# Optimization experiments

Hardware: AMD Instinct MI355X
Metric: run time of the kernel (lower is better)

Reference implementation:

```python
import jax, jax.numpy as jnp
import numpy as np

B, S, D, H = 2, 2048, 1024, 16
HD = D // H          # head dim = 64
BASE = 10000.0
SCALE = 1.0 / np.sqrt(HD)


def setup_inputs() -> dict:
    key = jax.random.key(0)
    ks = jax.random.split(key, 7)
    mk = lambda k, shp: (jax.random.normal(k, shp, dtype=jnp.float32) * 0.02)
    return {
        "hidden_states": jax.random.normal(ks[0], (B, S, D), dtype=jnp.float32),
        "Wq": mk(ks[1], (D, D)), "bq": jnp.zeros((D,), jnp.float32),
        "Wk": mk(ks[2], (D, D)), "bk": jnp.zeros((D,), jnp.float32),
        "Wv": mk(ks[3], (D, D)), "bv": jnp.zeros((D,), jnp.float32),
    }


def _rope_tables(seq_len, head_dim, dtype):
    # Intended RoPE: inv_freq over head_dim/2 frequencies.
    # (Original torch code has an off-by-2 indexing bug that makes it un-runnable
    #  for head_dim > 2; we implement the intended standard RoPE:
    #  inv_freq = base^{-arange(0, head_dim, 2)/head_dim}, length head_dim//2.)
    dim_half = head_dim // 2
    inv_freq = 1.0 / (BASE ** (jnp.arange(dim_half, dtype=dtype) / dim_half))
    ang = jnp.arange(seq_len, dtype=dtype)[:, None] * inv_freq[None, :]  # [S, dim_half]
    return jnp.sin(ang), jnp.cos(ang)


def _apply_rope(x, sin, cos):
    # x: [B, H, S, HD]; sin/cos: [S, HD//2]
    dim_half = x.shape[-1] // 2
    x1, x2 = x[..., :dim_half], x[..., dim_half:]
    sin = sin[None, None]  # [1,1,S,dim_half]
    cos = cos[None, None]
    return jnp.concatenate([x1 * cos - x2 * sin, x1 * sin + x2 * cos], axis=-1)


def reference(hidden_states, Wq, bq, Wk, bk, Wv, bv):
    b, s, d = hidden_states.shape
    # QKV projections (nn.Linear: x @ W.T + b), then split heads -> [B,H,S,HD]
    def proj(W, bias):
        y = jnp.einsum("bsd,ed->bse", hidden_states, W) + bias
        return y.reshape(b, s, H, HD).transpose(0, 2, 1, 3)

    q, k, v = proj(Wq, bq), proj(Wk, bk), proj(Wv, bv)

    sin, cos = _rope_tables(s, HD, hidden_states.dtype)
    q = _apply_rope(q, sin, cos)
    k = _apply_rope(k, sin, cos)

    # Non-causal SDPA, scale = 1/sqrt(head_dim), no mask, eval mode (no dropout)
    scores = jnp.einsum("bhqd,bhkd->bhqk", q, k) * SCALE
    probs = jax.nn.softmax(scores, axis=-1)
    ctx = jnp.einsum("bhqk,bhkd->bhqd", probs, v)

    # [B,H,S,HD] -> [B,S,D]
    return ctx.transpose(0, 2, 1, 3).reshape(b, s, d)
```

## Files before the change

kernel.cpp:

```cpp
#include <hip/hip_runtime.h>
#include <hip/hip_bf16.h>
#include <math.h>

#define B_  2
#define S_  2048
#define D_  1024
#define H_  16
#define HD_ 64
#define M_  (B_*S_)
#define N3  (3*D_)
#define K_  D_
#define LOG2E 1.44269504088896340736f

typedef unsigned short u16;
typedef __bf16 bf16x8 __attribute__((ext_vector_type(8)));
typedef float  f32x4  __attribute__((ext_vector_type(4)));
typedef float  f32x16 __attribute__((ext_vector_type(16)));
typedef unsigned short u16x4 __attribute__((ext_vector_type(4)));
typedef unsigned short u16x8 __attribute__((ext_vector_type(8)));
typedef unsigned int   u32x4v __attribute__((ext_vector_type(4)));

typedef const __attribute__((address_space(1))) unsigned int gu32;
typedef __attribute__((address_space(3)))       unsigned int lu32;

__device__ __forceinline__ void gload_lds16(const void* g, void* l) {
  __builtin_amdgcn_global_load_lds((gu32*)g, (lu32*)l, 16, 0, 0);
}

__device__ __forceinline__ u16 f2bf(float f) {
  unsigned u = __builtin_bit_cast(unsigned, f);
  u += 0x7fffu + ((u >> 16) & 1u);
  return (u16)(u >> 16);
}

__device__ __forceinline__ unsigned pk2(float lo, float hi) {
  unsigned d;
  asm("v_cvt_pk_bf16_f32 %0, %1, %2" : "=v"(d) : "v"(lo), "v"(hi));
  return d;
}

#define NPREP ((M_*D_/4 + 3*(D_*D_/4)) / 256)
__global__ void k_prep(const float* __restrict__ hs, const float* __restrict__ Wq,
                       const float* __restrict__ Wk, const float* __restrict__ Wv,
                       u16* __restrict__ Xb, u16* __restrict__ Wb,
                       float* __restrict__ sinT, float* __restrict__ cosT) {
  const int NX = M_*D_/4, NW = D_*D_/4, NTOT = NX + 3*NW;
  int i = blockIdx.x * blockDim.x + threadIdx.x;
  if (i < NTOT) {
    const float4* src; u16* dst; int off;
    if (i < NX)            { src = (const float4*)hs; dst = Xb;           off = i; }
    else if (i < NX+NW)    { src = (const float4*)Wq; dst = Wb;           off = i-NX; }
    else if (i < NX+2*NW)  { src = (const float4*)Wk; dst = Wb + D_*D_;   off = i-NX-NW; }
    else                   { src = (const float4*)Wv; dst = Wb + 2*D_*D_; off = i-NX-2*NW; }
    float4 v = src[off];
    ushort4 o; o.x = f2bf(v.x); o.y = f2bf(v.y); o.z = f2bf(v.z); o.w = f2bf(v.w);
    reinterpret_cast<ushort4*>(dst)[off] = o;
  } else {
    int gid = i - NTOT;
    int s = gid >> 5, j = gid & 31;
    float invf = (float)exp(-(double)j * (log(10000.0) / 32.0));
    float angf = (float)s * invf;
    double ang = (double)angf;
    sinT[gid] = (float)sin(ang);
    cosT[gid] = (float)cos(ang);
  }
}

#define BM 128
#define BN 128
#define BK 64

__global__ __launch_bounds__(256) void k_gemm(const u16* __restrict__ A,
                                              const u16* __restrict__ Bm,
                                              const float* __restrict__ bq,
                                              const float* __restrict__ bk,
                                              const float* __restrict__ bv,
                                              const float* __restrict__ sinT,
                                              const float* __restrict__ cosT,
                                              u16* __restrict__ Qo,
                                              u16* __restrict__ Ko,
                                              u16* __restrict__ Vt) {
  __shared__ alignas(16) u16 As[2][BM*BK];
  __shared__ alignas(16) u16 Bs[2][BN*BK];
  const int t = threadIdx.x;
  const int l = t & 63, w = t >> 6;
  const int wr = w >> 1, wc = w & 1;
  const int lr = l & 15, lg = l >> 4;

  const int lin = blockIdx.y * (N3/BN) + blockIdx.x;
  const int wk  = (lin & 7) * 96 + (lin >> 3);
  const int m0 = (wk / (N3/BN)) * BM, n0 = (wk % (N3/BN)) * BN;

  const u16* asrc[4]; const u16* bsrc[4];
#pragma unroll
  for (int i = 0; i < 4; ++i) {
    int chunk = i*256 + t;
    int row = chunk >> 3, kc = (chunk & 7) ^ (row & 7);
    asrc[i] = A  + (size_t)(m0+row)*K_ + kc*8;
    bsrc[i] = Bm + (size_t)(n0+row)*K_ + kc*8;
  }

  f32x4 acc[4][4] = {};

#pragma unroll
  for (int i = 0; i < 4; ++i) {
    int chunk = i*256 + t;
    gload_lds16(asrc[i], &As[0][chunk*8]);
    gload_lds16(bsrc[i], &Bs[0][chunk*8]);
  }
  __syncthreads();

  int cur = 0;
  for (int k0 = 0; k0 < K_; k0 += BK) {
    if (k0 + BK < K_) {
#pragma unroll
      for (int i = 0; i < 4; ++i) {
        int chunk = i*256 + t;
        gload_lds16(asrc[i] + k0 + BK, &As[cur^1][chunk*8]);
        gload_lds16(bsrc[i] + k0 + BK, &Bs[cur^1][chunk*8]);
      }
    }
#pragma unroll
    for (int ks = 0; ks < 2; ++ks) {
      bf16x8 a[4], b[4];
#pragma unroll
      for (int m = 0; m < 4; ++m) {
        int row = wr*64 + m*16 + lr;
        int g   = (ks*4 + lg) ^ (row & 7);
        a[m] = *reinterpret_cast<const bf16x8*>(&As[cur][row*BK + g*8]);
      }
#pragma unroll
      for (int n = 0; n < 4; ++n) {
        int row = wc*64 + n*16 + lr;
        int g   = (ks*4 + lg) ^ (row & 7);
        b[n] = *reinterpret_cast<const bf16x8*>(&Bs[cur][row*BK + g*8]);
      }
#pragma unroll
      for (int m = 0; m < 4; ++m)
#pragma unroll
        for (int n = 0; n < 4; ++n)
          acc[m][n] = __builtin_amdgcn_mfma_f32_16x16x32_bf16(a[m], b[n], acc[m][n], 0, 0, 0);
    }
    __syncthreads();
    cur ^= 1;
  }

  const int cw0  = n0 + wc*64;
  const int proj = cw0 >> 10;
  const int h    = (cw0 & (D_-1)) >> 6;
  const int b    = m0 >> 11;
  const int sb_  = (m0 & (S_-1)) + wr*64;

  if (proj < 2) {
    const float* bias = proj ? bk : bq;
    u16* dst = proj ? Ko : Qo;
    const float qs = proj ? 1.0f : 0.125f * LOG2E;
    float b1[2], b2[2];
#pragma unroll
    for (int n = 0; n < 2; ++n) {
      b1[n] = bias[h*HD_ + n*16 + lr];
      b2[n] = bias[h*HD_ + n*16 + lr + 32];
    }
#pragma unroll
    for (int m = 0; m < 4; ++m)
#pragma unroll
      for (int r = 0; r < 4; ++r) {
        int s = sb_ + m*16 + lg*4 + r;
        size_t orow = ((size_t)(b*H_ + h)*S_ + s)*HD_;
#pragma unroll
        for (int n = 0; n < 2; ++n) {
          int j = n*16 + lr;
          float x1 = acc[m][n][r]   + b1[n];
          float x2 = acc[m][n+2][r] + b2[n];
          float c  = cosT[(s<<5) + j], sn = sinT[(s<<5) + j];
          dst[orow + j]      = f2bf((x1*c - x2*sn) * qs);
          dst[orow + j + 32] = f2bf((x1*sn + x2*c) * qs);
        }
      }
  } else {
    float bb[4];
#pragma unroll
    for (int n = 0; n < 4; ++n) bb[n] = bv[h*HD_ + n*16 + lr];
    const int lgp = ((lg & 1) << 1) | (lg >> 1);
    const int pos0 = sb_ + lgp*4;
#pragma unroll
    for (int m = 0; m < 4; ++m)
#pragma unroll
      for (int n = 0; n < 4; ++n) {
        int hd = n*16 + lr;
        u16x4 o;
#pragma unroll
        for (int r = 0; r < 4; ++r) o[r] = f2bf(acc[m][n][r] + bb[n]);
        *reinterpret_cast<u16x4*>(Vt + ((size_t)(b*H_ + h)*HD_ + hd)*S_ + pos0 + m*16) = o;
      }
  }
}

#define QBW 32
#define NWV 4
#define QTT (QBW*NWV)
#define KTL 128
#define NTL (S_/KTL)

__global__ __launch_bounds__(256) void k_attn(const u16* __restrict__ Q,
                                              const u16* __restrict__ K,
                                              const u16* __restrict__ Vt,
                                              float* __restrict__ out) {
  __shared__ alignas(16) u16 Ks[2][KTL*HD_];
  __shared__ alignas(16) u16 Vs[2][HD_*KTL];
  __shared__ float lsums[NWV][QBW];
  const int t = threadIdx.x, l = t & 63, w = t >> 6;
  const int q32 = l & 31, hi = l >> 5;

  const int bid = blockIdx.x;
  const int work = (bid & 7) * 64 + (bid >> 3);
  const int bh = work >> 4;
  const int q0 = (work & 15) * QTT;

  const u16* Qg = Q  + ((size_t)bh*S_ + q0 + w*QBW)*HD_;
  const u16* Kg = K  + (size_t)bh*S_*HD_;
  const u16* Vg = Vt + (size_t)bh*HD_*S_;

  bf16x8 qf[4];
#pragma unroll
  for (int kt = 0; kt < 4; ++kt)
    qf[kt] = *reinterpret_cast<const bf16x8*>(Qg + (size_t)q32*HD_ + kt*16 + hi*8);

  f32x16 O0 = {}, O1 = {};
  float lp0 = 0.f, lp1 = 0.f, lp2 = 0.f, lp3 = 0.f;

  const u16* ksrc[4]; const u16* vsrc[4];
#pragma unroll
  for (int i = 0; i < 4; ++i) {
    int g  = t + 256*i;
    int kr = g >> 3,  kc = (g & 7)  ^ (kr & 7);
    ksrc[i] = Kg + (size_t)kr*HD_ + kc*8;
    int vr = g >> 4,  vc = (g & 15) ^ (vr & 15);
    vsrc[i] = Vg + (size_t)vr*S_ + vc*8;
  }

#pragma unroll
  for (int i = 0; i < 4; ++i) {
    gload_lds16(ksrc[i], &Ks[0][(t + 256*i)*8]);
    gload_lds16(vsrc[i], &Vs[0][(t + 256*i)*8]);
  }
  __syncthreads();

  int cur = 0;
  for (int tile = 0; tile < NTL; ++tile) {
    if (tile + 1 < NTL) {
#pragma unroll
      for (int i = 0; i < 4; ++i) {
        gload_lds16(ksrc[i] + (size_t)(tile+1)*KTL*HD_, &Ks[cur^1][(t + 256*i)*8]);
        gload_lds16(vsrc[i] + (tile+1)*KTL,             &Vs[cur^1][(t + 256*i)*8]);
      }
    }

#pragma unroll
    for (int half = 0; half < 2; ++half) {
      f32x16 d0 = {}, d1 = {};
      __builtin_amdgcn_s_setprio(1);
#pragma unroll
      for (int kt = 0; kt < 4; ++kt) {
        const int gsw = ((kt*2 + hi) ^ (q32 & 7)) * 8;
        bf16x8 k0 = *reinterpret_cast<const bf16x8*>(&Ks[cur][(half*64 + q32)*HD_ + gsw]);
        d0 = __builtin_amdgcn_mfma_f32_32x32x16_bf16(k0, qf[kt], d0, 0, 0, 0);
        bf16x8 k1 = *reinterpret_cast<const bf16x8*>(&Ks[cur][(half*64 + 32 + q32)*HD_ + gsw]);
        d1 = __builtin_amdgcn_mfma_f32_32x32x16_bf16(k1, qf[kt], d1, 0, 0, 0);
      }
      __builtin_amdgcn_s_setprio(0);

      unsigned pw[4][4];
#pragma unroll
      for (int c = 0; c < 4; ++c) {
        float e[8];
#pragma unroll
        for (int i = 0; i < 8; ++i) {
          float sv = (c < 2) ? d0[(c & 1)*8 + i] : d1[(c & 1)*8 + i];
          e[i] = __builtin_amdgcn_exp2f(sv);
        }
        lp0 += e[0] + e[4];
        lp1 += e[1] + e[5];
        lp2 += e[2] + e[6];
        lp3 += e[3] + e[7];
#pragma unroll
        for (int j = 0; j < 4; ++j) pw[c][j] = pk2(e[2*j], e[2*j+1]);
      }

      __builtin_amdgcn_s_setprio(1);
#pragma unroll
      for (int c = 0; c < 4; ++c) {
        u32x4v pv_ = {pw[c][0], pw[c][1], pw[c][2], pw[c][3]};
        bf16x8 pa = __builtin_bit_cast(bf16x8, pv_);
        const int gv = ((half*8 + c*2 + hi) ^ (q32 & 15)) * 8;
        bf16x8 v0 = *reinterpret_cast<const bf16x8*>(&Vs[cur][q32*KTL + gv]);
        O0 = __builtin_amdgcn_mfma_f32_32x32x16_bf16(pa, v0, O0, 0, 0, 0);
        bf16x8 v1 = *reinterpret_cast<const bf16x8*>(&Vs[cur][(32 + q32)*KTL + gv]);
        O1 = __builtin_amdgcn_mfma_f32_32x32x16_bf16(pa, v1, O1, 0, 0, 0);
      }
      __builtin_amdgcn_s_setprio(0);
    }

    __syncthreads();
    cur ^= 1;
  }

  float lsum = (lp0 + lp1) + (lp2 + lp3);
  lsum += __shfl_xor(lsum, 32);
  if (l < 32) lsums[w][l] = lsum;

  const int b = bh >> 4, h = bh & 15;
#pragma unroll
  for (int r = 0; r < 16; ++r) {
    int qrow = (r & 3) + 8*(r >> 2) + 4*hi;
    float inv = 1.f / lsums[w][qrow];
    size_t o = (size_t)(b*S_ + q0 + w*QBW + qrow)*D_ + h*HD_;
    out[o + q32]      = O0[r] * inv;
    out[o + 32 + q32] = O1[r] * inv;
  }
}

extern "C" void kernel_launch(void* const* d_in, const int* in_sizes, int n_in,
                              void* d_out, int out_size, void* d_ws, size_t ws_size,
                              hipStream_t stream) {
  const float* hs = (const float*)d_in[0];
  const float* Wq = (const float*)d_in[1];
  const float* bq = (const float*)d_in[2];
  const float* Wk = (const float*)d_in[3];
  const float* bk = (const float*)d_in[4];
  const float* Wv = (const float*)d_in[5];
  const float* bv = (const float*)d_in[6];
  float* out = (float*)d_out;

  char* ws = (char*)d_ws;
  u16*   Xb   = (u16*)  (ws);
  u16*   Wb   = (u16*)  (ws + 8388608);
  u16*   Qb   = (u16*)  (ws + 14680064);
  u16*   Kb   = (u16*)  (ws + 23068672);
  u16*   Vtb  = (u16*)  (ws + 31457280);
  float* sinT = (float*)(ws + 39845888);
  float* cosT = (float*)(ws + 40108032);

  k_prep<<<NPREP + 256, 256, 0, stream>>>(hs, Wq, Wk, Wv, Xb, Wb, sinT, cosT);
  k_gemm<<<dim3(N3/BN, M_/BM), 256, 0, stream>>>(Xb, Wb, bq, bk, bv, sinT, cosT, Qb, Kb, Vtb);
  k_attn<<<512, 256, 0, stream>>>(Qb, Kb, Vtb, out);
}
```

Measured before the change: 172.7 us.

## Split attention over two key halves with a separate reduction kernel

Attention work is split across two key/value halves, doubling the grid to 1024 blocks. Each block handles 1024 keys in 64-wide tiles with a new LDS swizzle, and writes unnormalised partial outputs and row sums. A new reduction kernel adds the two partials and divides by the combined sum. The aim is more parallelism and occupancy (launch bounds 4, smaller LDS), at the cost of an extra full-size fp32 output round trip and one more launch. The RoPE table computation also switches from double to single-precision sin and cos.

```diff
diff --git a/kernel.cpp b/kernel.cpp
--- a/kernel.cpp
+++ b/kernel.cpp
@@ -59,10 +59,9 @@
     int gid = i - NTOT;
     int s = gid >> 5, j = gid & 31;
     float invf = (float)exp(-(double)j * (log(10000.0) / 32.0));
-    float angf = (float)s * invf;
-    double ang = (double)angf;
-    sinT[gid] = (float)sin(ang);
-    cosT[gid] = (float)cos(ang);
+    float ang  = (float)s * invf;
+    sinT[gid] = sinf(ang);
+    cosT[gid] = cosf(ang);
   }
 }
 
@@ -199,27 +198,29 @@
 #define QBW 32
 #define NWV 4
 #define QTT (QBW*NWV)
-#define KTL 128
-#define NTL (S_/KTL)
-
-__global__ __launch_bounds__(256) void k_attn(const u16* __restrict__ Q,
-                                              const u16* __restrict__ K,
-                                              const u16* __restrict__ Vt,
-                                              float* __restrict__ out) {
+#define KTL 64
+#define NTL 16
+
+__global__ __launch_bounds__(256, 4) void k_attn(const u16* __restrict__ Q,
+                                                 const u16* __restrict__ K,
+                                                 const u16* __restrict__ Vt,
+                                                 float* __restrict__ out,
+                                                 float* __restrict__ Op2,
+                                                 float* __restrict__ Lp) {
   __shared__ alignas(16) u16 Ks[2][KTL*HD_];
   __shared__ alignas(16) u16 Vs[2][HD_*KTL];
-  __shared__ float lsums[NWV][QBW];
   const int t = threadIdx.x, l = t & 63, w = t >> 6;
   const int q32 = l & 31, hi = l >> 5;
 
   const int bid = blockIdx.x;
-  const int work = (bid & 7) * 64 + (bid >> 3);
-  const int bh = work >> 4;
+  const int work = (bid & 7) * 128 + (bid >> 3);
+  const int bh = work >> 5;
+  const int ks = (work >> 4) & 1;
   const int q0 = (work & 15) * QTT;
 
   const u16* Qg = Q  + ((size_t)bh*S_ + q0 + w*QBW)*HD_;
-  const u16* Kg = K  + (size_t)bh*S_*HD_;
-  const u16* Vg = Vt + (size_t)bh*HD_*S_;
+  const u16* Kg = K  + ((size_t)bh*S_ + ks*1024)*HD_;
+  const u16* Vg = Vt + (size_t)bh*HD_*S_ + ks*1024;
 
   bf16x8 qf[4];
 #pragma unroll
@@ -229,77 +230,77 @@
   f32x16 O0 = {}, O1 = {};
   float lp0 = 0.f, lp1 = 0.f, lp2 = 0.f, lp3 = 0.f;
 
-  const u16* ksrc[4]; const u16* vsrc[4];
-#pragma unroll
-  for (int i = 0; i < 4; ++i) {
+  const u16 *ksrc[2], *vsrc[2];
+#pragma unroll
+  for (int i = 0; i < 2; ++i) {
     int g  = t + 256*i;
-    int kr = g >> 3,  kc = (g & 7)  ^ (kr & 7);
-    ksrc[i] = Kg + (size_t)kr*HD_ + kc*8;
-    int vr = g >> 4,  vc = (g & 15) ^ (vr & 15);
-    vsrc[i] = Vg + (size_t)vr*S_ + vc*8;
-  }
-
-#pragma unroll
-  for (int i = 0; i < 4; ++i) {
+    int r_ = g >> 4;
+    int kg = (g & 15) ^ (r_ & 15);
+    ksrc[i] = Kg + (size_t)(r_*2 + (kg >> 3))*HD_ + (kg & 7)*8;
+    vsrc[i] = Vg + (size_t)(r_*2 + (kg >> 3))*S_  + (kg & 7)*8;
+  }
+
+#pragma unroll
+  for (int i = 0; i < 2; ++i) {
     gload_lds16(ksrc[i], &Ks[0][(t + 256*i)*8]);
     gload_lds16(vsrc[i], &Vs[0][(t + 256*i)*8]);
   }
   __syncthreads();
+
+  const int rk = q32 >> 1;
+  const int kb = (q32 & 1) << 3;
 
   int cur = 0;
   for (int tile = 0; tile < NTL; ++tile) {
     if (tile + 1 < NTL) {
 #pragma unroll
-      for (int i = 0; i < 4; ++i) {
+      for (int i = 0; i < 2; ++i) {
         gload_lds16(ksrc[i] + (size_t)(tile+1)*KTL*HD_, &Ks[cur^1][(t + 256*i)*8]);
         gload_lds16(vsrc[i] + (tile+1)*KTL,             &Vs[cur^1][(t + 256*i)*8]);
       }
     }
 
-#pragma unroll
-    for (int half = 0; half < 2; ++half) {
-      f32x16 d0 = {}, d1 = {};
-      __builtin_amdgcn_s_setprio(1);
-#pragma unroll
-      for (int kt = 0; kt < 4; ++kt) {
-        const int gsw = ((kt*2 + hi) ^ (q32 & 7)) * 8;
-        bf16x8 k0 = *reinterpret_cast<const bf16x8*>(&Ks[cur][(half*64 + q32)*HD_ + gsw]);
-        d0 = __builtin_amdgcn_mfma_f32_32x32x16_bf16(k0, qf[kt], d0, 0, 0, 0);
-        bf16x8 k1 = *reinterpret_cast<const bf16x8*>(&Ks[cur][(half*64 + 32 + q32)*HD_ + gsw]);
-        d1 = __builtin_amdgcn_mfma_f32_32x32x16_bf16(k1, qf[kt], d1, 0, 0, 0);
-      }
-      __builtin_amdgcn_s_setprio(0);
-
-      unsigned pw[4][4];
-#pragma unroll
-      for (int c = 0; c < 4; ++c) {
-        float e[8];
-#pragma unroll
-        for (int i = 0; i < 8; ++i) {
-          float sv = (c < 2) ? d0[(c & 1)*8 + i] : d1[(c & 1)*8 + i];
-          e[i] = __builtin_amdgcn_exp2f(sv);
-        }
-        lp0 += e[0] + e[4];
-        lp1 += e[1] + e[5];
-        lp2 += e[2] + e[6];
-        lp3 += e[3] + e[7];
-#pragma unroll
-        for (int j = 0; j < 4; ++j) pw[c][j] = pk2(e[2*j], e[2*j+1]);
-      }
-
-      __builtin_amdgcn_s_setprio(1);
-#pragma unroll
-      for (int c = 0; c < 4; ++c) {
-        u32x4v pv_ = {pw[c][0], pw[c][1], pw[c][2], pw[c][3]};
-        bf16x8 pa = __builtin_bit_cast(bf16x8, pv_);
-        const int gv = ((half*8 + c*2 + hi) ^ (q32 & 15)) * 8;
-        bf16x8 v0 = *reinterpret_cast<const bf16x8*>(&Vs[cur][q32*KTL + gv]);
-        O0 = __builtin_amdgcn_mfma_f32_32x32x16_bf16(pa, v0, O0, 0, 0, 0);
-        bf16x8 v1 = *reinterpret_cast<const bf16x8*>(&Vs[cur][(32 + q32)*KTL + gv]);
-        O1 = __builtin_amdgcn_mfma_f32_32x32x16_bf16(pa, v1, O1, 0, 0, 0);
-      }
-      __builtin_amdgcn_s_setprio(0);
-    }
+    f32x16 d0 = {}, d1 = {};
+    __builtin_amdgcn_s_setprio(1);
+#pragma unroll
+    for (int kt = 0; kt < 4; ++kt) {
+      const int g0 = (kb | (kt*2 + hi)) ^ rk;
+      bf16x8 k0 = *reinterpret_cast<const bf16x8*>(&Ks[cur][(rk*16 + g0)*8]);
+      d0 = __builtin_amdgcn_mfma_f32_32x32x16_bf16(k0, qf[kt], d0, 0, 0, 0);
+      bf16x8 k1 = *reinterpret_cast<const bf16x8*>(&Ks[cur][((16 + rk)*16 + g0)*8]);
+      d1 = __builtin_amdgcn_mfma_f32_32x32x16_bf16(k1, qf[kt], d1, 0, 0, 0);
+    }
+    __builtin_amdgcn_s_setprio(0);
+
+    unsigned pw[4][4];
+#pragma unroll
+    for (int c = 0; c < 4; ++c) {
+      float e[8];
+#pragma unroll
+      for (int i = 0; i < 8; ++i) {
+        float sv = (c < 2) ? d0[(c & 1)*8 + i] : d1[(c & 1)*8 + i];
+        e[i] = __builtin_amdgcn_exp2f(sv);
+      }
+      lp0 += e[0] + e[4];
+      lp1 += e[1] + e[5];
+      lp2 += e[2] + e[6];
+      lp3 += e[3] + e[7];
+#pragma unroll
+      for (int j = 0; j < 4; ++j) pw[c][j] = pk2(e[2*j], e[2*j+1]);
+    }
+
+    __builtin_amdgcn_s_setprio(1);
+#pragma unroll
+    for (int c = 0; c < 4; ++c) {
+      u32x4v pv_ = {pw[c][0], pw[c][1], pw[c][2], pw[c][3]};
+      bf16x8 pa = __builtin_bit_cast(bf16x8, pv_);
+      const int gv = (kb | (c*2 + hi)) ^ rk;
+      bf16x8 v0 = *reinterpret_cast<const bf16x8*>(&Vs[cur][(rk*16 + gv)*8]);
+      O0 = __builtin_amdgcn_mfma_f32_32x32x16_bf16(pa, v0, O0, 0, 0, 0);
+      bf16x8 v1 = *reinterpret_cast<const bf16x8*>(&Vs[cur][((16 + rk)*16 + gv)*8]);
+      O1 = __builtin_amdgcn_mfma_f32_32x32x16_bf16(pa, v1, O1, 0, 0, 0);
+    }
+    __builtin_amdgcn_s_setprio(0);
 
     __syncthreads();
     cur ^= 1;
@@ -307,17 +308,33 @@
 
   float lsum = (lp0 + lp1) + (lp2 + lp3);
   lsum += __shfl_xor(lsum, 32);
-  if (l < 32) lsums[w][l] = lsum;
-
+  if (l < 32) Lp[ks*65536 + bh*2048 + q0 + w*QBW + l] = lsum;
+
+  float* Od = ks ? Op2 : out;
   const int b = bh >> 4, h = bh & 15;
 #pragma unroll
   for (int r = 0; r < 16; ++r) {
     int qrow = (r & 3) + 8*(r >> 2) + 4*hi;
-    float inv = 1.f / lsums[w][qrow];
     size_t o = (size_t)(b*S_ + q0 + w*QBW + qrow)*D_ + h*HD_;
-    out[o + q32]      = O0[r] * inv;
-    out[o + 32 + q32] = O1[r] * inv;
-  }
+    Od[o + q32]      = O0[r];
+    Od[o + 32 + q32] = O1[r];
+  }
+}
+
+__global__ __launch_bounds__(256) void k_red(float* __restrict__ out,
+                                             const float* __restrict__ Op2,
+                                             const float* __restrict__ Lp) {
+  int i4 = blockIdx.x * 256 + threadIdx.x;
+  float4 a = reinterpret_cast<const float4*>(out)[i4];
+  float4 b = reinterpret_cast<const float4*>(Op2)[i4];
+  int bs = i4 >> 8;
+  int h  = (i4 & 255) >> 4;
+  int li = ((bs >> 11)*16 + h)*2048 + (bs & 2047);
+  float inv = 1.f / (Lp[li] + Lp[65536 + li]);
+  float4 r;
+  r.x = (a.x + b.x) * inv; r.y = (a.y + b.y) * inv;
+  r.z = (a.z + b.z) * inv; r.w = (a.w + b.w) * inv;
+  reinterpret_cast<float4*>(out)[i4] = r;
 }
 
 extern "C" void kernel_launch(void* const* d_in, const int* in_sizes, int n_in,
@@ -333,15 +350,18 @@
   float* out = (float*)d_out;
 
   char* ws = (char*)d_ws;
+  float* Op2  = (float*)(ws);
+  float* Lp   = (float*)(ws + 16777216);
   u16*   Xb   = (u16*)  (ws);
   u16*   Wb   = (u16*)  (ws + 8388608);
-  u16*   Qb   = (u16*)  (ws + 14680064);
-  u16*   Kb   = (u16*)  (ws + 23068672);
-  u16*   Vtb  = (u16*)  (ws + 31457280);
-  float* sinT = (float*)(ws + 39845888);
-  float* cosT = (float*)(ws + 40108032);
+  u16*   Qb   = (u16*)  (ws + 17301504);
+  u16*   Kb   = (u16*)  (ws + 25690112);
+  u16*   Vtb  = (u16*)  (ws + 34078720);
+  float* sinT = (float*)(ws + 42467328);
+  float* cosT = (float*)(ws + 42729472);
 
   k_prep<<<NPREP + 256, 256, 0, stream>>>(hs, Wq, Wk, Wv, Xb, Wb, sinT, cosT);
   k_gemm<<<dim3(N3/BN, M_/BM), 256, 0, stream>>>(Xb, Wb, bq, bk, bv, sinT, cosT, Qb, Kb, Vtb);
-  k_attn<<<512, 256, 0, stream>>>(Qb, Kb, Vtb, out);
-}
+  k_attn<<<1024, 256, 0, stream>>>(Qb, Kb, Vtb, out, Op2, Lp);
+  k_red<<<4096, 256, 0, stream>>>(out, Op2, Lp);
+}
```

Result: slower. 181.3 us (+5.0%).
